# Performance work log

Measured on AMD Instinct MI355X. Metric: run time of the kernel, lower is better.

Reference implementation:

```python
import jax, jax.numpy as jnp
import numpy as np

B, S, H, L, NH, OUT = 64, 512, 512, 2, 8, 1
HD = H // NH
SKIP_INTERVAL = 2
EPS = 1e-5


def ln(x, g, b):
    m = x.mean(-1, keepdims=True)
    v = x.var(-1, keepdims=True)
    return (x - m) / jnp.sqrt(v + EPS) * g + b


def setup_inputs() -> dict:
    key = jax.random.key(0)
    ks = iter(jax.random.split(key, 64))
    def nrm(shape, s=0.02):
        return jax.random.normal(next(ks), shape, jnp.float32) * s
    inp = {
        'x': jax.random.normal(next(ks), (B, S, H), jnp.float32),
        # stacked per-layer LSTM params (input_size == hidden_size == H)
        'Wi': nrm((L, 4 * H, H)), 'bi': jnp.zeros((L, 4 * H), jnp.float32).at[:, H:2 * H].set(1.0),
        'Wh': nrm((L, 4 * H, H)), 'bh': jnp.zeros((L, 4 * H), jnp.float32).at[:, H:2 * H].set(1.0),
        'g_in': jnp.ones((L, 4 * H), jnp.float32), 'b_in': jnp.zeros((L, 4 * H), jnp.float32),
        'g_hid': jnp.ones((L, 4 * H), jnp.float32), 'b_hid': jnp.zeros((L, 4 * H), jnp.float32),
        'g_cell': jnp.ones((L, H), jnp.float32), 'b_cell': jnp.zeros((L, H), jnp.float32),
        # highway per layer
        'hw_Wt': nrm((L, H, H)), 'hw_bt': jnp.zeros((L, H), jnp.float32),
        'hw_Wc': nrm((L, H, H)), 'hw_bc': jnp.full((L, H), -1.0, jnp.float32),
        'hw_Wh': nrm((L, H, H)), 'hw_bh': jnp.zeros((L, H), jnp.float32),
        # attention
        'Wq': nrm((H, H)), 'bq': jnp.zeros((H,), jnp.float32),
        'Wk': nrm((H, H)), 'bk': jnp.zeros((H,), jnp.float32),
        'Wv': nrm((H, H)), 'bv': jnp.zeros((H,), jnp.float32),
        'Wo': nrm((H, H)), 'bo': jnp.zeros((H,), jnp.float32),
        'att_g': jnp.ones((H,), jnp.float32), 'att_b': jnp.zeros((H,), jnp.float32),
        # output norm + projection head
        'on_g': jnp.ones((H,), jnp.float32), 'on_b': jnp.zeros((H,), jnp.float32),
        'Wp1': nrm((H // 2, H)), 'bp1': jnp.zeros((H // 2,), jnp.float32),
        'Wp2': nrm((OUT, H // 2)), 'bp2': jnp.zeros((OUT,), jnp.float32),
    }
    return inp


def _forward(x, Wi, bi, Wh, bh, g_in, b_in, g_hid, b_hid, g_cell, b_cell,
             hw_Wt, hw_bt, hw_Wc, hw_bc, hw_Wh, hw_bh,
             Wq, bq, Wk, bk, Wv, bv, Wo, bo, att_g, att_b,
             on_g, on_b, Wp1, bp1, Wp2, bp2):
    def lstm_layer(seq, l):
        # precompute input projection + its LayerNorm for all timesteps: [B,S,4H]
        ip = ln(jnp.einsum('bsh,gh->bsg', seq, Wi[l]) + bi[l], g_in[l], b_in[l])
        def step(carry, ip_t):
            h, c = carry
            hp = ln(h @ Wh[l].T + bh[l], g_hid[l], b_hid[l])
            i_, f_, g_, o_ = jnp.split(ip_t + hp, 4, axis=-1)
            c = jax.nn.sigmoid(f_) * c + jax.nn.sigmoid(i_) * jnp.tanh(g_)
            h = jax.nn.sigmoid(o_) * jnp.tanh(ln(c, g_cell[l], b_cell[l]))
            return (h, c), h
        h0 = jnp.zeros((seq.shape[0], H), seq.dtype)
        _, hs = jax.lax.scan(step, (h0, h0), jnp.swapaxes(ip, 0, 1))
        return jnp.swapaxes(hs, 0, 1)  # [B,S,H]

    seq = x
    for l in range(L):
        h_seq = lstm_layer(seq, l)
        # highway network
        tg = jax.nn.sigmoid(h_seq @ hw_Wt[l].T + hw_bt[l])
        cg = jax.nn.sigmoid(h_seq @ hw_Wc[l].T + hw_bc[l])
        tr = jax.nn.relu(h_seq @ hw_Wh[l].T + hw_bh[l])
        h_seq = tg * tr + cg * h_seq
        # skip connection every SKIP_INTERVAL layers
        if l > 0 and (l + 1) % SKIP_INTERVAL == 0:
            h_seq = h_seq + seq
        seq = h_seq

    # multi-head self-attention with residual + LayerNorm
    def heads(y):
        return jnp.swapaxes(y.reshape(B, S, NH, HD), 1, 2)  # [B,NH,S,HD]
    q = heads(seq @ Wq.T + bq)
    k = heads(seq @ Wk.T + bk)
    v = heads(seq @ Wv.T + bv)
    scale = 1.0 / float(np.sqrt(HD))
    scores = jnp.einsum('bnqd,bnkd->bnqk', q, k) * scale
    aw = jax.nn.softmax(scores, axis=-1)
    ctx = jnp.einsum('bnqk,bnkd->bnqd', aw, v)
    ctx = jnp.swapaxes(ctx, 1, 2).reshape(B, S, H)
    att = ln(ctx @ Wo.T + bo + seq, att_g, att_b)

    # last timestep -> output norm -> MLP head
    last = ln(att[:, -1], on_g, on_b)
    hmid = jax.nn.relu(last @ Wp1.T + bp1)
    return hmid @ Wp2.T + bp2  # [B, OUT]


def reference(x, Wi, bi, Wh, bh, g_in, b_in, g_hid, b_hid, g_cell, b_cell,
              hw_Wt, hw_bt, hw_Wc, hw_bc, hw_Wh, hw_bh,
              Wq, bq, Wk, bk, Wv, bv, Wo, bo, att_g, att_b,
              on_g, on_b, Wp1, bp1, Wp2, bp2):
    return _forward(x, Wi, bi, Wh, bh, g_in, b_in, g_hid, b_hid, g_cell, b_cell,
                    hw_Wt, hw_bt, hw_Wc, hw_bc, hw_Wh, hw_bh,
                    Wq, bq, Wk, bk, Wv, bv, Wo, bo, att_g, att_b,
                    on_g, on_b, Wp1, bp1, Wp2, bp2)
```

## Files before the change

kernel.cpp:

```cpp
#include <hip/hip_runtime.h>

#define EPS_LN 1e-5f

static constexpr int Bn  = 64;
static constexpr int Sn  = 512;
static constexpr int Hn  = 512;
static constexpr int G4n = 2048;

typedef unsigned int uint32;
typedef unsigned long long uint64;
typedef _Float16 h2v __attribute__((ext_vector_type(2)));

__device__ __forceinline__ float sigf(float x)     { return 1.0f / (1.0f + __expf(-x)); }
__device__ __forceinline__ float tanhfast(float x) { return 1.0f - 2.0f / (1.0f + __expf(2.0f * x)); }

__device__ __forceinline__ float dot2h(uint32 w, uint32 h, float acc) {
#if defined(__has_builtin)
#if __has_builtin(__builtin_amdgcn_fdot2)
  return __builtin_amdgcn_fdot2(__builtin_bit_cast(h2v, w), __builtin_bit_cast(h2v, h), acc, false);
#define DOT2_DONE 1
#endif
#endif
#ifndef DOT2_DONE
  h2v wv = __builtin_bit_cast(h2v, w);
  h2v hv = __builtin_bit_cast(h2v, h);
  return acc + (float)wv.x * (float)hv.x + (float)wv.y * (float)hv.y;
#endif
}
__device__ __forceinline__ uint32 packh2(float a, float b) {
  h2v v; v.x = (_Float16)a; v.y = (_Float16)b;
  return __builtin_bit_cast(uint32, v);
}

__device__ __forceinline__ float blk_sum(float v, float* sm, int tid) {
#pragma unroll
  for (int o = 32; o; o >>= 1) v += __shfl_down(v, o, 64);
  __syncthreads();
  if ((tid & 63) == 0) sm[tid >> 6] = v;
  __syncthreads();
  return sm[0] + sm[1] + sm[2] + sm[3];
}
__device__ __forceinline__ float blk_max(float v, float* sm, int tid) {
#pragma unroll
  for (int o = 32; o; o >>= 1) v = fmaxf(v, __shfl_down(v, o, 64));
  __syncthreads();
  if ((tid & 63) == 0) sm[tid >> 6] = v;
  __syncthreads();
  return fmaxf(fmaxf(sm[0], sm[1]), fmaxf(sm[2], sm[3]));
}

__device__ __forceinline__ void blk_sum4_w8(float& a, float& b, float& c, float& d,
                                            float* sm, int tid) {
#pragma unroll
  for (int o = 32; o; o >>= 1) {
    a += __shfl_down(a, o, 64);
    b += __shfl_down(b, o, 64);
    c += __shfl_down(c, o, 64);
    d += __shfl_down(d, o, 64);
  }
  __syncthreads();
  if ((tid & 63) == 0) {
    float4 v; v.x = a; v.y = b; v.z = c; v.w = d;
    *(float4*)&sm[(tid >> 6) * 4] = v;
  }
  __syncthreads();
  float ra = 0.f, rb = 0.f, rc = 0.f, rd = 0.f;
#pragma unroll
  for (int w = 0; w < 8; ++w) {
    float4 v = *(const float4*)&sm[w * 4];
    ra += v.x; rb += v.y; rc += v.z; rd += v.w;
  }
  a = ra; b = rb; c = rc; d = rd;
}

__global__ __launch_bounds__(256) void wh_pack_k(
    const float* __restrict__ Wh, uint32* __restrict__ WhP)
{
  __shared__ float tile[32][33];
  const int l = blockIdx.z;
  const int k0 = blockIdx.x * 32;
  const int n0 = blockIdx.y * 32;
  const int row = threadIdx.x >> 5, col = threadIdx.x & 31;
  const float* src = Wh + (long)l * G4n * Hn;
  uint32* dst = WhP + (long)l * 256 * G4n;
#pragma unroll
  for (int rr = 0; rr < 4; ++rr) {
    int nn = row + rr * 8;
    tile[nn][col] = src[(long)(n0 + nn) * Hn + k0 + col];
  }
  __syncthreads();
#pragma unroll
  for (int rr = 0; rr < 2; ++rr) {
    int kpl = row + rr * 8;
    int kp = (k0 >> 1) + kpl;
    dst[(long)kp * G4n + n0 + col] = packh2(tile[col][2*kpl], tile[col][2*kpl+1]);
  }
}

__global__ void init_zbuf_k(uint64* zbuf)
{
  long i = (long)blockIdx.x * 512 + threadIdx.x;
  zbuf[i] = 0ULL;
}

__global__ __launch_bounds__(256) void gemm_ip_k(
    const float* __restrict__ A,
    const float* __restrict__ Bw,
    const float* __restrict__ bias,
    float* __restrict__ C,
    int s0)
{
  __shared__ __align__(16) uint32 Ah[8][128];
  __shared__ __align__(16) uint32 Bh[8][128];
  const int tid = threadIdx.x;
  const long m0 = (long)blockIdx.y * 128;
  const long n0 = (long)blockIdx.x * 128;
  const int tx = tid & 15, ty = tid >> 4;
  const int lrow = tid >> 1;
  const int lc0  = (tid & 1) * 8;
  const int kb   = (tid & 1) * 4;
  float acc[8][8];
#pragma unroll
  for (int i = 0; i < 8; ++i)
#pragma unroll
    for (int j = 0; j < 8; ++j) acc[i][j] = 0.f;

  const long r  = m0 + lrow;
  const long b  = r & 63;
  const long sl = r >> 6;
  const float* Arow = A + (b * Sn + s0 + sl) * Hn;
  const float* Brow = Bw + (n0 + lrow) * 512L;

  float4 a0 = *(const float4*)(Arow + lc0);
  float4 a1 = *(const float4*)(Arow + lc0 + 4);
  float4 b0 = *(const float4*)(Brow + lc0);
  float4 b1 = *(const float4*)(Brow + lc0 + 4);

  for (int k0 = 0; k0 < 512; k0 += 16) {
    __syncthreads();
    Ah[kb+0][lrow] = packh2(a0.x, a0.y);
    Ah[kb+1][lrow] = packh2(a0.z, a0.w);
    Ah[kb+2][lrow] = packh2(a1.x, a1.y);
    Ah[kb+3][lrow] = packh2(a1.z, a1.w);
    Bh[kb+0][lrow] = packh2(b0.x, b0.y);
    Bh[kb+1][lrow] = packh2(b0.z, b0.w);
    Bh[kb+2][lrow] = packh2(b1.x, b1.y);
    Bh[kb+3][lrow] = packh2(b1.z, b1.w);
    __syncthreads();
    if (k0 + 16 < 512) {
      a0 = *(const float4*)(Arow + k0 + 16 + lc0);
      a1 = *(const float4*)(Arow + k0 + 16 + lc0 + 4);
      b0 = *(const float4*)(Brow + k0 + 16 + lc0);
      b1 = *(const float4*)(Brow + k0 + 16 + lc0 + 4);
    }
#pragma unroll
    for (int kp = 0; kp < 8; ++kp) {
      uint32 a8[8], b8[8];
      *(uint4*)&a8[0] = *(const uint4*)&Ah[kp][ty*8];
      *(uint4*)&a8[4] = *(const uint4*)&Ah[kp][ty*8+4];
      *(uint4*)&b8[0] = *(const uint4*)&Bh[kp][tx*8];
      *(uint4*)&b8[4] = *(const uint4*)&Bh[kp][tx*8+4];
#pragma unroll
      for (int i = 0; i < 8; ++i)
#pragma unroll
        for (int j = 0; j < 8; ++j) acc[i][j] = dot2h(a8[i], b8[j], acc[i][j]);
    }
  }
#pragma unroll
  for (int i = 0; i < 8; ++i) {
    long m = m0 + ty*8 + i;
    float* crow = C + m * 2048L + n0 + tx*8;
    const float* br = bias + n0 + tx*8;
    float4 o0, o1;
    o0.x = acc[i][0]+br[0]; o0.y = acc[i][1]+br[1]; o0.z = acc[i][2]+br[2]; o0.w = acc[i][3]+br[3];
    o1.x = acc[i][4]+br[4]; o1.y = acc[i][5]+br[5]; o1.z = acc[i][6]+br[6]; o1.w = acc[i][7]+br[7];
    *(float4*)crow = o0; *(float4*)(crow+4) = o1;
  }
}

__global__ __launch_bounds__(256) void hw_fused_k(
    const float* __restrict__ A,
    const float* __restrict__ Wt, const float* __restrict__ bt,
    const float* __restrict__ Wc, const float* __restrict__ bc,
    const float* __restrict__ Wh3, const float* __restrict__ bh3,
    float* __restrict__ seqout,
    int skip)
{
  __shared__ __align__(16) uint32 Ah[8][128];
  __shared__ __align__(16) uint32 Bh[3][8][68];
  const int tid = threadIdx.x;
  const long m0 = (long)blockIdx.y * 128;
  const int n0 = blockIdx.x * 64;
  const int tx = tid & 7;
  const int ty = tid >> 3;
  const int lrow = tid >> 1;
  const int lc0  = (tid & 1) * 8;
  const int kbA  = (tid & 1) * 4;
  const int brow = tid >> 2;
  const int bk0  = (tid & 3) * 4;
  const int kbB  = (tid & 3) * 2;

  float accT[4][8], accC[4][8], accH[4][8];
#pragma unroll
  for (int i = 0; i < 4; ++i)
#pragma unroll
    for (int j = 0; j < 8; ++j) { accT[i][j] = 0.f; accC[i][j] = 0.f; accH[i][j] = 0.f; }

  const float* Arow = A + (m0 + lrow) * 512;
  const long boff = (long)(n0 + brow) * 512 + bk0;

  float4 a0 = *(const float4*)(Arow + lc0);
  float4 a1 = *(const float4*)(Arow + lc0 + 4);
  float4 wt4 = *(const float4*)(Wt  + boff);
  float4 wc4 = *(const float4*)(Wc  + boff);
  float4 wh4 = *(const float4*)(Wh3 + boff);

  for (int k0 = 0; k0 < 512; k0 += 16) {
    __syncthreads();
    Ah[kbA+0][lrow] = packh2(a0.x, a0.y);
    Ah[kbA+1][lrow] = packh2(a0.z, a0.w);
    Ah[kbA+2][lrow] = packh2(a1.x, a1.y);
    Ah[kbA+3][lrow] = packh2(a1.z, a1.w);
    Bh[0][kbB+0][brow] = packh2(wt4.x, wt4.y);
    Bh[0][kbB+1][brow] = packh2(wt4.z, wt4.w);
    Bh[1][kbB+0][brow] = packh2(wc4.x, wc4.y);
    Bh[1][kbB+1][brow] = packh2(wc4.z, wc4.w);
    Bh[2][kbB+0][brow] = packh2(wh4.x, wh4.y);
    Bh[2][kbB+1][brow] = packh2(wh4.z, wh4.w);
    __syncthreads();
    if (k0 + 16 < 512) {
      a0 = *(const float4*)(Arow + k0 + 16 + lc0);
      a1 = *(const float4*)(Arow + k0 + 16 + lc0 + 4);
      wt4 = *(const float4*)(Wt  + boff + k0 + 16);
      wc4 = *(const float4*)(Wc  + boff + k0 + 16);
      wh4 = *(const float4*)(Wh3 + boff + k0 + 16);
    }
#pragma unroll
    for (int kp = 0; kp < 8; ++kp) {
      uint32 a4[4];
      *(uint4*)&a4[0] = *(const uint4*)&Ah[kp][ty*4];
      {
        uint32 b8[8];
        *(uint4*)&b8[0] = *(const uint4*)&Bh[0][kp][tx*8];
        *(uint4*)&b8[4] = *(const uint4*)&Bh[0][kp][tx*8+4];
#pragma unroll
        for (int i = 0; i < 4; ++i)
#pragma unroll
          for (int j = 0; j < 8; ++j) accT[i][j] = dot2h(a4[i], b8[j], accT[i][j]);
      }
      {
        uint32 b8[8];
        *(uint4*)&b8[0] = *(const uint4*)&Bh[1][kp][tx*8];
        *(uint4*)&b8[4] = *(const uint4*)&Bh[1][kp][tx*8+4];
#pragma unroll
        for (int i = 0; i < 4; ++i)
#pragma unroll
          for (int j = 0; j < 8; ++j) accC[i][j] = dot2h(a4[i], b8[j], accC[i][j]);
      }
      {
        uint32 b8[8];
        *(uint4*)&b8[0] = *(const uint4*)&Bh[2][kp][tx*8];
        *(uint4*)&b8[4] = *(const uint4*)&Bh[2][kp][tx*8+4];
#pragma unroll
        for (int i = 0; i < 4; ++i)
#pragma unroll
          for (int j = 0; j < 8; ++j) accH[i][j] = dot2h(a4[i], b8[j], accH[i][j]);
      }
    }
  }

  float btr[8], bcr[8], bhr[8];
#pragma unroll
  for (int j = 0; j < 8; ++j) {
    btr[j] = bt[n0 + tx*8 + j];
    bcr[j] = bc[n0 + tx*8 + j];
    bhr[j] = bh3[n0 + tx*8 + j];
  }
#pragma unroll
  for (int i = 0; i < 4; ++i) {
    const long m = m0 + ty*4 + i;
    const float* hrow = A + m * 512 + n0 + tx*8;
    float* srow = seqout + m * 512 + n0 + tx*8;
    float4 h0 = *(const float4*)hrow;
    float4 h1 = *(const float4*)(hrow + 4);
    float hv[8] = {h0.x,h0.y,h0.z,h0.w,h1.x,h1.y,h1.z,h1.w};
    float sv[8] = {0,0,0,0,0,0,0,0};
    if (skip) {
      float4 s0 = *(const float4*)srow;
      float4 s1 = *(const float4*)(srow + 4);
      sv[0]=s0.x; sv[1]=s0.y; sv[2]=s0.z; sv[3]=s0.w;
      sv[4]=s1.x; sv[5]=s1.y; sv[6]=s1.z; sv[7]=s1.w;
    }
    float o[8];
#pragma unroll
    for (int j = 0; j < 8; ++j) {
      const float t1 = accT[i][j] + btr[j];
      const float t2 = accC[i][j] + bcr[j];
      const float t3 = accH[i][j] + bhr[j];
      o[j] = sigf(t1) * fmaxf(t3, 0.f) + sigf(t2) * hv[j] + sv[j];
    }
    float4 o0, o1;
    o0.x=o[0]; o0.y=o[1]; o0.z=o[2]; o0.w=o[3];
    o1.x=o[4]; o1.y=o[5]; o1.z=o[6]; o1.w=o[7];
    *(float4*)srow = o0; *(float4*)(srow + 4) = o1;
  }
}

__global__ __launch_bounds__(256) void gemm_m64_k(
    const float* __restrict__ A, long lda,
    const float* __restrict__ Bw,
    const float* __restrict__ bias,
    float* __restrict__ P,
    int N, int K)
{
  __shared__ float As[64][64];
  __shared__ float Bs[64][64];
  const int tid = threadIdx.x;
  const int n0 = blockIdx.x * 64;
  const int kc = blockIdx.y;
  const int Kc = K / gridDim.y;
  const int tx = tid & 15, ty = tid >> 4;
  const int row = tid >> 2, q = tid & 3;
  float acc[4][4];
#pragma unroll
  for (int i = 0; i < 4; ++i)
#pragma unroll
    for (int j = 0; j < 4; ++j) acc[i][j] = 0.f;

  for (int k0 = kc * Kc; k0 < kc * Kc + Kc; k0 += 64) {
    float4 a[4], b[4];
#pragma unroll
    for (int c = 0; c < 4; ++c) {
      a[c] = *(const float4*)(A  + (long)row * lda       + k0 + q*16 + c*4);
      b[c] = *(const float4*)(Bw + (long)(n0 + row) * K  + k0 + q*16 + c*4);
    }
    __syncthreads();
#pragma unroll
    for (int c = 0; c < 4; ++c) {
      int kb = q*16 + c*4;
      As[kb+0][row]=a[c].x; As[kb+1][row]=a[c].y; As[kb+2][row]=a[c].z; As[kb+3][row]=a[c].w;
      Bs[kb+0][row]=b[c].x; Bs[kb+1][row]=b[c].y; Bs[kb+2][row]=b[c].z; Bs[kb+3][row]=b[c].w;
    }
    __syncthreads();
#pragma unroll
    for (int kk = 0; kk < 64; ++kk) {
      float4 av = *(const float4*)&As[kk][ty*4];
      float4 bv = *(const float4*)&Bs[kk][tx*4];
      float am[4] = {av.x, av.y, av.z, av.w};
      float bm[4] = {bv.x, bv.y, bv.z, bv.w};
#pragma unroll
      for (int i = 0; i < 4; ++i)
#pragma unroll
        for (int j = 0; j < 4; ++j) acc[i][j] += am[i] * bm[j];
    }
  }
#pragma unroll
  for (int i = 0; i < 4; ++i) {
    int m = ty*4 + i;
    float* pr = P + ((long)kc * 64 + m) * N + n0 + tx*4;
#pragma unroll
    for (int j = 0; j < 4; ++j) {
      float bb = bias ? bias[n0 + tx*4 + j] : 0.f;
      pr[j] = acc[i][j] + bb;
    }
  }
}

__global__ __launch_bounds__(512, 2) void lstm_seqz_k(
    const uint32* __restrict__ WhP,
    const float* __restrict__ bh,
    const float* __restrict__ ipc,
    const float* __restrict__ g_hid, const float* __restrict__ b_hid,
    const float* __restrict__ g_cell, const float* __restrict__ b_cell,
    float* __restrict__ hst, float* __restrict__ cst,
    float* __restrict__ hseq,
    uint64* __restrict__ zbuf,
    int t0, int nsteps, int gbase)
{
  const int blk = blockIdx.x;
  const int g   = blk & 31;
  const int kq  = blk >> 5;
  const int tid = threadIdx.x;
  const int b0  = g*2, b1 = g*2 + 1;
  const int r   = tid >> 1;
  const int kh  = tid & 1;
  __shared__ __align__(16) uint32 hp0[264];
  __shared__ __align__(16) uint32 hp1[264];
  __shared__ float sm[32];

  uint4 wreg[32];
  {
    const uint32* base = WhP + (long)(kh * 128) * 2048 + (kq*256 + r);
#pragma unroll
    for (int i = 0; i < 32; ++i) {
      wreg[i].x = base[(long)(4*i + 0) * 2048];
      wreg[i].y = base[(long)(4*i + 1) * 2048];
      wreg[i].z = base[(long)(4*i + 2) * 2048];
      wreg[i].w = base[(long)(4*i + 3) * 2048];
    }
  }

  float bhr[4], ghr[4], bhir[4];
#pragma unroll
  for (int q = 0; q < 4; ++q) {
    bhr[q]  = bh[q*512 + tid];
    ghr[q]  = g_hid[q*512 + tid];
    bhir[q] = b_hid[q*512 + tid];
  }
  const float gcv = g_cell[tid];
  const float bcv = b_cell[tid];
  float c0 = cst[b0*512 + tid];
  float c1 = cst[b1*512 + tid];
  float h0 = hst[b0*512 + tid];
  float h1 = hst[b1*512 + tid];

  {
    const float p0 = __shfl_xor(h0, 1, 64);
    const float p1 = __shfl_xor(h1, 1, 64);
    if (!(tid & 1)) {
      const int j = tid >> 1;
      const int jj = (j < 128) ? j : j + 4;
      hp0[jj] = packh2(h0, p0);
      hp1[jj] = packh2(h1, p1);
    }
  }
  __syncthreads();

  const long myword = (long)(kq*256 + r) * 2 + kh;
  const uint32* hb0 = hp0 + kh * 132;
  const uint32* hb1 = hp1 + kh * 132;

  for (int ts = 0; ts < nsteps; ++ts) {
    const int gstep = gbase + ts;
    const uint32 tagw = (uint32)gstep;
    uint64* zp = zbuf + (long)(gstep & 1) * 131072 + (long)g * 4096;

    const float* iprow0 = ipc + ((long)ts * 64 + b0) * 2048 + tid;
    const float* iprow1 = ipc + ((long)ts * 64 + b1) * 2048 + tid;
    float ip0[4], ip1[4];
#pragma unroll
    for (int q = 0; q < 4; ++q) { ip0[q] = iprow0[q*512]; ip1[q] = iprow1[q*512]; }

    float a0 = 0.f, a1 = 0.f;
#pragma unroll
    for (int i = 0; i < 32; ++i) {
      const uint4 w  = wreg[i];
      const uint4 hv0 = *(const uint4*)&hb0[4*i];
      const uint4 hv1 = *(const uint4*)&hb1[4*i];
      a0 = dot2h(w.x, hv0.x, a0); a0 = dot2h(w.y, hv0.y, a0);
      a0 = dot2h(w.z, hv0.z, a0); a0 = dot2h(w.w, hv0.w, a0);
      a1 = dot2h(w.x, hv1.x, a1); a1 = dot2h(w.y, hv1.y, a1);
      a1 = dot2h(w.z, hv1.z, a1); a1 = dot2h(w.w, hv1.w, a1);
    }
    a0 += __shfl_xor(a0, 1, 64);
    a1 += __shfl_xor(a1, 1, 64);

    {
      const float zval = kh ? a1 : a0;
      const uint64 w = ((uint64)tagw << 32) | (uint64)__builtin_bit_cast(uint32, zval);
      __hip_atomic_store(zp + myword, w, __ATOMIC_RELAXED, __HIP_MEMORY_SCOPE_AGENT);
    }

    float z0[4], z1[4];
    {
      uint64 v0[4], v1[4];
      int pend = 0xff;
      while (pend) {
#pragma unroll
        for (int q = 0; q < 4; ++q) {
          const long base = (long)(q*512 + tid) * 2;
          if (pend & (1 << q)) {
            uint64 w = __hip_atomic_load(zp + base, __ATOMIC_RELAXED, __HIP_MEMORY_SCOPE_AGENT);
            if ((uint32)(w >> 32) == tagw) { v0[q] = w; pend &= ~(1 << q); }
          }
          if (pend & (16 << q)) {
            uint64 w = __hip_atomic_load(zp + base + 1, __ATOMIC_RELAXED, __HIP_MEMORY_SCOPE_AGENT);
            if ((uint32)(w >> 32) == tagw) { v1[q] = w; pend &= ~(16 << q); }
          }
        }
        if (pend) __builtin_amdgcn_s_sleep(2);
      }
#pragma unroll
      for (int q = 0; q < 4; ++q) {
        z0[q] = __builtin_bit_cast(float, (uint32)v0[q]) + bhr[q];
        z1[q] = __builtin_bit_cast(float, (uint32)v1[q]) + bhr[q];
      }
    }

    float s10 = z0[0]+z0[1]+z0[2]+z0[3];
    float s20 = z0[0]*z0[0] + z0[1]*z0[1] + z0[2]*z0[2] + z0[3]*z0[3];
    float s11 = z1[0]+z1[1]+z1[2]+z1[3];
    float s21 = z1[0]*z1[0] + z1[1]*z1[1] + z1[2]*z1[2] + z1[3]*z1[3];
    blk_sum4_w8(s10, s20, s11, s21, sm, tid);
    const float m0 = s10 * (1.f/2048.f);
    const float r0 = rsqrtf(s20 * (1.f/2048.f) - m0*m0 + EPS_LN);
    const float m1 = s11 * (1.f/2048.f);
    const float r1 = rsqrtf(s21 * (1.f/2048.f) - m1*m1 + EPS_LN);

    const float gi0 = ip0[0] + (z0[0] - m0) * r0 * ghr[0] + bhir[0];
    const float gf0 = ip0[1] + (z0[1] - m0) * r0 * ghr[1] + bhir[1];
    const float gg0 = ip0[2] + (z0[2] - m0) * r0 * ghr[2] + bhir[2];
    const float go0 = ip0[3] + (z0[3] - m0) * r0 * ghr[3] + bhir[3];
    const float gi1 = ip1[0] + (z1[0] - m1) * r1 * ghr[0] + bhir[0];
    const float gf1 = ip1[1] + (z1[1] - m1) * r1 * ghr[1] + bhir[1];
    const float gg1 = ip1[2] + (z1[2] - m1) * r1 * ghr[2] + bhir[2];
    const float go1 = ip1[3] + (z1[3] - m1) * r1 * ghr[3] + bhir[3];

    c0 = sigf(gf0) * c0 + sigf(gi0) * tanhfast(gg0);
    c1 = sigf(gf1) * c1 + sigf(gi1) * tanhfast(gg1);

    float t10 = c0, t20 = c0*c0, t11 = c1, t21 = c1*c1;
    blk_sum4_w8(t10, t20, t11, t21, sm, tid);
    const float n0 = t10 * (1.f/512.f);
    const float q0r = rsqrtf(t20 * (1.f/512.f) - n0*n0 + EPS_LN);
    const float n1 = t11 * (1.f/512.f);
    const float q1r = rsqrtf(t21 * (1.f/512.f) - n1*n1 + EPS_LN);
    h0 = sigf(go0) * tanhfast((c0 - n0) * q0r * gcv + bcv);
    h1 = sigf(go1) * tanhfast((c1 - n1) * q1r * gcv + bcv);

    if (kq == 0) {
      hseq[((long)b0 * Sn + t0 + ts) * Hn + tid] = h0;
      hseq[((long)b1 * Sn + t0 + ts) * Hn + tid] = h1;
    }

    const float p0 = __shfl_xor(h0, 1, 64);
    const float p1 = __shfl_xor(h1, 1, 64);
    if (!(tid & 1)) {
      const int j = tid >> 1;
      const int jj = (j < 128) ? j : j + 4;
      hp0[jj] = packh2(h0, p0);
      hp1[jj] = packh2(h1, p1);
    }
    __syncthreads();
  }
  if (kq == 0) {
    hst[b0*512 + tid] = h0; hst[b1*512 + tid] = h1;
    cst[b0*512 + tid] = c0; cst[b1*512 + tid] = c1;
  }
}

__global__ __launch_bounds__(256) void ln_rows_k(
    float* __restrict__ X, const float* __restrict__ g, const float* __restrict__ bt)
{
  const long row = blockIdx.x;
  float* xr = X + row * 2048L;
  const int tid = threadIdx.x;
  __shared__ float sm[4];
  float4 v0 = *(float4*)(xr + tid*8);
  float4 v1 = *(float4*)(xr + tid*8 + 4);
  float s1 = v0.x+v0.y+v0.z+v0.w + v1.x+v1.y+v1.z+v1.w;
  float s2 = v0.x*v0.x+v0.y*v0.y+v0.z*v0.z+v0.w*v0.w
           + v1.x*v1.x+v1.y*v1.y+v1.z*v1.z+v1.w*v1.w;
  s1 = blk_sum(s1, sm, tid);
  s2 = blk_sum(s2, sm, tid);
  const float mean = s1 * (1.f/2048.f);
  const float rstd = rsqrtf(s2 * (1.f/2048.f) - mean*mean + EPS_LN);
  const int base = tid*8;
  float vals[8] = {v0.x,v0.y,v0.z,v0.w,v1.x,v1.y,v1.z,v1.w};
#pragma unroll
  for (int c = 0; c < 8; ++c)
    xr[base + c] = (vals[c] - mean) * rstd * g[base + c] + bt[base + c];
}

__global__ void init_hc_k(float* h, float* c)
{
  int i = blockIdx.x * 256 + threadIdx.x;
  h[i] = 0.f; c[i] = 0.f;
}

__global__ __launch_bounds__(256) void qkh_k(
    const float* __restrict__ qlst, const float* __restrict__ Wk,
    const float* __restrict__ bk,
    float* __restrict__ qkh, float* __restrict__ qbk)
{
  const int hd = blockIdx.x, cg = blockIdx.y;
  const int b = threadIdx.x & 63, sc = threadIdx.x >> 6;
  const int col0 = cg * 128 + sc * 32;
  float qreg[64];
  const float* qp = qlst + b*512 + hd*64;
#pragma unroll
  for (int j4 = 0; j4 < 16; ++j4) {
    float4 v = *(const float4*)(qp + j4*4);
    qreg[j4*4+0]=v.x; qreg[j4*4+1]=v.y; qreg[j4*4+2]=v.z; qreg[j4*4+3]=v.w;
  }
  float acc[32];
#pragma unroll
  for (int c = 0; c < 32; ++c) acc[c] = 0.f;
  for (int j = 0; j < 64; ++j) {
    float qv = qreg[j];
    const float* wr = Wk + (long)(hd*64 + j)*512 + col0;
#pragma unroll
    for (int c4 = 0; c4 < 8; ++c4) {
      float4 w = *(const float4*)(wr + c4*4);
      acc[c4*4+0] = __builtin_fmaf(qv, w.x, acc[c4*4+0]);
      acc[c4*4+1] = __builtin_fmaf(qv, w.y, acc[c4*4+1]);
      acc[c4*4+2] = __builtin_fmaf(qv, w.z, acc[c4*4+2]);
      acc[c4*4+3] = __builtin_fmaf(qv, w.w, acc[c4*4+3]);
    }
  }
  float* op = qkh + ((long)b*8 + hd)*512 + col0;
#pragma unroll
  for (int c4 = 0; c4 < 8; ++c4) {
    float4 o;
    o.x = acc[c4*4+0]; o.y = acc[c4*4+1]; o.z = acc[c4*4+2]; o.w = acc[c4*4+3];
    *(float4*)(op + c4*4) = o;
  }
  if (cg == 0 && sc == 0) {
    float s = 0.f;
    for (int j = 0; j < 64; ++j) s += qreg[j] * bk[hd*64 + j];
    qbk[b*8 + hd] = s;
  }
}

__global__ __launch_bounds__(256) void attn2_k(
    const float* __restrict__ seq,
    const float* __restrict__ qkh,
    const float* __restrict__ qbk,
    float* __restrict__ u)
{
  const int b = blockIdx.x, hd = blockIdx.y, tid = threadIdx.x;
  __shared__ __align__(16) float qk[512];
  __shared__ float p[512];
  __shared__ float sm[4];
  qk[tid]       = qkh[((long)b*8 + hd)*512 + tid];
  qk[tid + 256] = qkh[((long)b*8 + hd)*512 + tid + 256];
  __syncthreads();
  const float bias = qbk[b*8 + hd];

  float loc[2]; float mx = -3.0e38f;
#pragma unroll
  for (int v = 0; v < 2; ++v) {
    int s = tid + v*256;
    const float4* sr = (const float4*)(seq + ((long)b*512 + s)*512);
    const float4* qv4 = (const float4*)qk;
    float d = 0.f;
    for (int k4 = 0; k4 < 128; ++k4) {
      float4 sv = sr[k4], qv = qv4[k4];
      d += sv.x*qv.x + sv.y*qv.y + sv.z*qv.z + sv.w*qv.w;
    }
    d = (d + bias) * 0.125f;
    loc[v] = d; mx = fmaxf(mx, d);
  }
  const float M = blk_max(mx, sm, tid);
  float sum = 0.f;
#pragma unroll
  for (int v = 0; v < 2; ++v) {
    int s = tid + v*256;
    float e = __expf(loc[v] - M);
    p[s] = e; sum += e;
  }
  const float SM = blk_sum(sum, sm, tid);
  const float inv = 1.f / SM;

  float u0 = 0.f, u1 = 0.f;
  for (int s = 0; s < 512; ++s) {
    float ps = p[s];
    const float* srow = seq + ((long)b*512 + s)*512;
    u0 = __builtin_fmaf(ps, srow[tid], u0);
    u1 = __builtin_fmaf(ps, srow[tid + 256], u1);
  }
  u[((long)b*8 + hd)*512 + tid]       = u0 * inv;
  u[((long)b*8 + hd)*512 + tid + 256] = u1 * inv;
}

__global__ __launch_bounds__(256) void ctxv_k(
    const float* __restrict__ u, const float* __restrict__ Wv,
    const float* __restrict__ bv, float* __restrict__ ctx)
{
  const int b = blockIdx.x, tid = threadIdx.x;
  __shared__ __align__(16) float ul[8*512];
  for (int i = tid; i < 4096; i += 256) ul[i] = u[(long)b*4096 + i];
  __syncthreads();
#pragma unroll
  for (int v = 0; v < 2; ++v) {
    int n = tid + v*256;
    int hd = n >> 6;
    const float4* wr = (const float4*)(Wv + (long)n*512);
    const float4* uv = (const float4*)&ul[hd*512];
    float acc = 0.f;
    for (int k4 = 0; k4 < 128; ++k4) {
      float4 w = wr[k4], x = uv[k4];
      acc += w.x*x.x + w.y*x.y + w.z*x.z + w.w*x.w;
    }
    ctx[b*512 + n] = acc + bv[n];
  }
}

__global__ __launch_bounds__(256) void head_k(
    const float* __restrict__ ctx,
    const float* __restrict__ Wo, const float* __restrict__ bo,
    const float* __restrict__ seq,
    const float* __restrict__ att_g, const float* __restrict__ att_b,
    const float* __restrict__ on_g, const float* __restrict__ on_b,
    const float* __restrict__ Wp1, const float* __restrict__ bp1,
    const float* __restrict__ Wp2, const float* __restrict__ bp2,
    float* __restrict__ out)
{
  const int b = blockIdx.x, tid = threadIdx.x;
  __shared__ __align__(16) float cs[512];
  __shared__ __align__(16) float buf[512];
  __shared__ float sm[4];
  cs[tid]       = ctx[b*512 + tid];
  cs[tid + 256] = ctx[b*512 + tid + 256];
  __syncthreads();

  const float* srow = seq + ((long)b*512 + 511) * 512;
  float o[2];
#pragma unroll
  for (int v = 0; v < 2; ++v) {
    int j = tid + v*256;
    const float4* w4 = (const float4*)(Wo + (long)j * 512);
    const float4* c4 = (const float4*)cs;
    float acc = 0.f;
    for (int kx = 0; kx < 128; ++kx) {
      float4 w = w4[kx], c = c4[kx];
      acc += w.x*c.x + w.y*c.y + w.z*c.z + w.w*c.w;
    }
    o[v] = acc + bo[j] + srow[j];
  }
  float s1 = o[0] + o[1], s2 = o[0]*o[0] + o[1]*o[1];
  s1 = blk_sum(s1, sm, tid); s2 = blk_sum(s2, sm, tid);
  float m1 = s1 * (1.f/512.f);
  float r1 = rsqrtf(s2 * (1.f/512.f) - m1*m1 + EPS_LN);
  float a[2];
#pragma unroll
  for (int v = 0; v < 2; ++v) {
    int j = tid + v*256;
    a[v] = (o[v] - m1) * r1 * att_g[j] + att_b[j];
  }
  s1 = a[0] + a[1]; s2 = a[0]*a[0] + a[1]*a[1];
  s1 = blk_sum(s1, sm, tid); s2 = blk_sum(s2, sm, tid);
  float m2 = s1 * (1.f/512.f);
  float r2 = rsqrtf(s2 * (1.f/512.f) - m2*m2 + EPS_LN);
#pragma unroll
  for (int v = 0; v < 2; ++v) {
    int j = tid + v*256;
    buf[j] = (a[v] - m2) * r2 * on_g[j] + on_b[j];
  }
  __syncthreads();

  const float4* w1 = (const float4*)(Wp1 + (long)tid * 512);
  const float4* b4 = (const float4*)buf;
  float acc = 0.f;
  for (int kx = 0; kx < 128; ++kx) {
    float4 w = w1[kx], c = b4[kx];
    acc += w.x*c.x + w.y*c.y + w.z*c.z + w.w*c.w;
  }
  float mid = fmaxf(acc + bp1[tid], 0.f);
  float contrib = mid * Wp2[tid];
  float tot = blk_sum(contrib, sm, tid);
  if (tid == 0) out[b] = tot + bp2[0];
}

extern "C" void kernel_launch(void* const* d_in, const int* in_sizes, int n_in,
                              void* d_out, int out_size, void* d_ws, size_t ws_size,
                              hipStream_t stream)
{
  const float* x     = (const float*)d_in[0];
  const float* Wi    = (const float*)d_in[1];
  const float* bi    = (const float*)d_in[2];
  const float* Wh    = (const float*)d_in[3];
  const float* bh    = (const float*)d_in[4];
  const float* g_in  = (const float*)d_in[5];
  const float* b_in  = (const float*)d_in[6];
  const float* g_hid = (const float*)d_in[7];
  const float* b_hid = (const float*)d_in[8];
  const float* g_cell= (const float*)d_in[9];
  const float* b_cell= (const float*)d_in[10];
  const float* hwWt  = (const float*)d_in[11];
  const float* hwbt  = (const float*)d_in[12];
  const float* hwWc  = (const float*)d_in[13];
  const float* hwbc  = (const float*)d_in[14];
  const float* hwWh  = (const float*)d_in[15];
  const float* hwbh  = (const float*)d_in[16];
  const float* Wq    = (const float*)d_in[17];
  const float* bq    = (const float*)d_in[18];
  const float* Wk    = (const float*)d_in[19];
  const float* bk    = (const float*)d_in[20];
  const float* Wv    = (const float*)d_in[21];
  const float* bv    = (const float*)d_in[22];
  const float* Wo    = (const float*)d_in[23];
  const float* bo    = (const float*)d_in[24];
  const float* att_g = (const float*)d_in[25];
  const float* att_b = (const float*)d_in[26];
  const float* on_g  = (const float*)d_in[27];
  const float* on_b  = (const float*)d_in[28];
  const float* Wp1   = (const float*)d_in[29];
  const float* bp1   = (const float*)d_in[30];
  const float* Wp2   = (const float*)d_in[31];
  const float* bp2   = (const float*)d_in[32];
  float* out = (float*)d_out;

  const long SEQF = (long)Bn * Sn * Hn;
  const long WHPF = 2L * 256 * G4n;
  const long ZBF  = 2L * 32 * 2048 * 2;
  const long wsF  = (long)(ws_size / 4);

  float* ws   = (float*)d_ws;
  float* seq  = ws;
  float* hseq = seq  + SEQF;
  uint32* WhP = (uint32*)(hseq + SEQF);
  uint64* zbuf = (uint64*)(hseq + SEQF + WHPF);
  float* hst  = hseq + SEQF + WHPF + 2*ZBF;
  float* cst  = hst  + 32768L;
  float* qlst = cst  + 32768L;
  float* ctx  = qlst + 32768L;
  float* qkh  = ctx  + 32768L;
  float* qbk  = qkh  + 262144L;
  float* uat  = qbk  + 1024L;
  float* ipc  = uat  + 262144L;
  const long baseF = (ipc - ws);

  int TCH = 128;
  while (TCH > 16 && baseF + (long)TCH * 64 * 2048 > wsF) TCH >>= 1;

  wh_pack_k<<<dim3(16, 64, 2), 256, 0, stream>>>(Wh, WhP);
  init_zbuf_k<<<512, 512, 0, stream>>>(zbuf);

  const int NCH = Sn / TCH;
  const int MROWS = TCH * 64;
  const int NMCH = (Bn * Sn) / MROWS;

  for (int l = 0; l < 2; ++l) {
    const float* seqin = (l == 0) ? x : seq;
    init_hc_k<<<128, 256, 0, stream>>>(hst, cst);
    for (int c = 0; c < NCH; ++c) {
      const int s0 = c * TCH;
      gemm_ip_k<<<dim3(16, TCH/2), 256, 0, stream>>>(seqin, Wi + (long)l*G4n*Hn, bi + l*G4n, ipc, s0);
      ln_rows_k<<<TCH*64, 256, 0, stream>>>(ipc, g_in + l*G4n, b_in + l*G4n);
      lstm_seqz_k<<<256, 512, 0, stream>>>(WhP + (long)l*256*G4n, bh + l*G4n, ipc,
          g_hid + l*G4n, b_hid + l*G4n, g_cell + l*Hn, b_cell + l*Hn,
          hst, cst, hseq, zbuf, s0, TCH, l*Sn + s0 + 1);
    }
    for (int mc = 0; mc < NMCH; ++mc) {
      const long m0 = (long)mc * MROWS;
      hw_fused_k<<<dim3(8, MROWS/128), 256, 0, stream>>>(
          hseq + m0*512,
          hwWt + (long)l*Hn*Hn, hwbt + l*Hn,
          hwWc + (long)l*Hn*Hn, hwbc + l*Hn,
          hwWh + (long)l*Hn*Hn, hwbh + l*Hn,
          seq + m0*512, (l == 0) ? 0 : 1);
    }
  }

  gemm_m64_k<<<dim3(8, 1), 256, 0, stream>>>(seq + 511L*512, 512L*512, Wq, bq, qlst, 512, 512);
  qkh_k<<<dim3(8, 4), 256, 0, stream>>>(qlst, Wk, bk, qkh, qbk);
  attn2_k<<<dim3(64, 8), 256, 0, stream>>>(seq, qkh, qbk, uat);
  ctxv_k<<<64, 256, 0, stream>>>(uat, Wv, bv, ctx);
  head_k<<<64, 256, 0, stream>>>(ctx, Wo, bo, seq, att_g, att_b, on_g, on_b, Wp1, bp1, Wp2, bp2, out);
}
```

Measured before the change: 9.184 ms.

## Store input projection as fp16 and apply input LayerNorm inside LSTM kernel

The input-projection GEMM now writes packed fp16 pairs instead of fp32. The separate LayerNorm pass is replaced by a stats-only kernel that writes a per-row mean and rstd. The recurrent LSTM kernel reads the fp16 values and applies the normalization with g_in/b_in inline, which removes a full read-modify-write pass and halves the per-step loads of the projection buffer. The smaller buffer also lets the time chunk grow to 256, so there are fewer chunk launches, at the cost of fp16 rounding of pre-normalization gate inputs.

Measured after the change: 9.067 ms. About the same (-1.3%).

```diff
diff --git a/kernel.cpp b/kernel.cpp
--- a/kernel.cpp
+++ b/kernel.cpp
@@ -107,7 +107,7 @@
     const float* __restrict__ A,
     const float* __restrict__ Bw,
     const float* __restrict__ bias,
-    float* __restrict__ C,
+    uint32* __restrict__ C,
     int s0)
 {
   __shared__ __align__(16) uint32 Ah[8][128];
@@ -169,12 +169,41 @@
 #pragma unroll
   for (int i = 0; i < 8; ++i) {
     long m = m0 + ty*8 + i;
-    float* crow = C + m * 2048L + n0 + tx*8;
+    uint32* crow = C + m * 1024 + (n0 >> 1) + tx*4;
     const float* br = bias + n0 + tx*8;
-    float4 o0, o1;
-    o0.x = acc[i][0]+br[0]; o0.y = acc[i][1]+br[1]; o0.z = acc[i][2]+br[2]; o0.w = acc[i][3]+br[3];
-    o1.x = acc[i][4]+br[4]; o1.y = acc[i][5]+br[5]; o1.z = acc[i][6]+br[6]; o1.w = acc[i][7]+br[7];
-    *(float4*)crow = o0; *(float4*)(crow+4) = o1;
+    uint4 o;
+    o.x = packh2(acc[i][0]+br[0], acc[i][1]+br[1]);
+    o.y = packh2(acc[i][2]+br[2], acc[i][3]+br[3]);
+    o.z = packh2(acc[i][4]+br[4], acc[i][5]+br[5]);
+    o.w = packh2(acc[i][6]+br[6], acc[i][7]+br[7]);
+    *(uint4*)crow = o;
+  }
+}
+
+__global__ __launch_bounds__(256) void ipstats_k(
+    const uint32* __restrict__ X, float* __restrict__ st)
+{
+  const long row = blockIdx.x;
+  const uint32* xr = X + row * 1024;
+  const int tid = threadIdx.x;
+  __shared__ float sm[4];
+  uint4 w = *(const uint4*)(xr + tid*4);
+  h2v a = __builtin_bit_cast(h2v, w.x);
+  h2v b = __builtin_bit_cast(h2v, w.y);
+  h2v c = __builtin_bit_cast(h2v, w.z);
+  h2v d = __builtin_bit_cast(h2v, w.w);
+  float v[8] = {(float)a.x,(float)a.y,(float)b.x,(float)b.y,
+                (float)c.x,(float)c.y,(float)d.x,(float)d.y};
+  float s1 = 0.f, s2 = 0.f;
+#pragma unroll
+  for (int i = 0; i < 8; ++i) { s1 += v[i]; s2 += v[i]*v[i]; }
+  s1 = blk_sum(s1, sm, tid);
+  s2 = blk_sum(s2, sm, tid);
+  if (tid == 0) {
+    const float mean = s1 * (1.f/2048.f);
+    const float rstd = rsqrtf(s2 * (1.f/2048.f) - mean*mean + EPS_LN);
+    st[row*2]     = mean;
+    st[row*2 + 1] = rstd;
   }
 }
 
@@ -369,7 +398,9 @@
 __global__ __launch_bounds__(512, 2) void lstm_seqz_k(
     const uint32* __restrict__ WhP,
     const float* __restrict__ bh,
-    const float* __restrict__ ipc,
+    const uint32* __restrict__ ipc,
+    const float* __restrict__ ipstats,
+    const float* __restrict__ g_in, const float* __restrict__ b_in,
     const float* __restrict__ g_hid, const float* __restrict__ b_hid,
     const float* __restrict__ g_cell, const float* __restrict__ b_cell,
     float* __restrict__ hst, float* __restrict__ cst,
@@ -400,12 +431,14 @@
     }
   }
 
-  float bhr[4], ghr[4], bhir[4];
+  float bhr[4], ghr[4], bhir[4], ginr[4], binr[4];
 #pragma unroll
   for (int q = 0; q < 4; ++q) {
     bhr[q]  = bh[q*512 + tid];
     ghr[q]  = g_hid[q*512 + tid];
     bhir[q] = b_hid[q*512 + tid];
+    ginr[q] = g_in[q*512 + tid];
+    binr[q] = b_in[q*512 + tid];
   }
   const float gcv = g_cell[tid];
   const float bcv = b_cell[tid];
@@ -435,11 +468,20 @@
     const uint32 tagw = (uint32)gstep;
     uint64* zp = zbuf + (long)(gstep & 1) * 131072 + (long)g * 4096;
 
-    const float* iprow0 = ipc + ((long)ts * 64 + b0) * 2048 + tid;
-    const float* iprow1 = ipc + ((long)ts * 64 + b1) * 2048 + tid;
+    const uint32* iprow0 = ipc + ((long)ts * 64 + b0) * 1024 + (tid >> 1);
+    const uint32* iprow1 = ipc + ((long)ts * 64 + b1) * 1024 + (tid >> 1);
+    const float2 st0 = *(const float2*)(ipstats + ((long)ts * 64 + b0) * 2);
+    const float2 st1 = *(const float2*)(ipstats + ((long)ts * 64 + b1) * 2);
     float ip0[4], ip1[4];
 #pragma unroll
-    for (int q = 0; q < 4; ++q) { ip0[q] = iprow0[q*512]; ip1[q] = iprow1[q*512]; }
+    for (int q = 0; q < 4; ++q) {
+      h2v v0 = __builtin_bit_cast(h2v, iprow0[q*256]);
+      h2v v1 = __builtin_bit_cast(h2v, iprow1[q*256]);
+      const float r0 = kh ? (float)v0.y : (float)v0.x;
+      const float r1 = kh ? (float)v1.y : (float)v1.x;
+      ip0[q] = (r0 - st0.x) * st0.y * ginr[q] + binr[q];
+      ip1[q] = (r1 - st1.x) * st1.y * ginr[q] + binr[q];
+    }
 
     float a0 = 0.f, a1 = 0.f;
 #pragma unroll
@@ -537,29 +579,6 @@
     hst[b0*512 + tid] = h0; hst[b1*512 + tid] = h1;
     cst[b0*512 + tid] = c0; cst[b1*512 + tid] = c1;
   }
-}
-
-__global__ __launch_bounds__(256) void ln_rows_k(
-    float* __restrict__ X, const float* __restrict__ g, const float* __restrict__ bt)
-{
-  const long row = blockIdx.x;
-  float* xr = X + row * 2048L;
-  const int tid = threadIdx.x;
-  __shared__ float sm[4];
-  float4 v0 = *(float4*)(xr + tid*8);
-  float4 v1 = *(float4*)(xr + tid*8 + 4);
-  float s1 = v0.x+v0.y+v0.z+v0.w + v1.x+v1.y+v1.z+v1.w;
-  float s2 = v0.x*v0.x+v0.y*v0.y+v0.z*v0.z+v0.w*v0.w
-           + v1.x*v1.x+v1.y*v1.y+v1.z*v1.z+v1.w*v1.w;
-  s1 = blk_sum(s1, sm, tid);
-  s2 = blk_sum(s2, sm, tid);
-  const float mean = s1 * (1.f/2048.f);
-  const float rstd = rsqrtf(s2 * (1.f/2048.f) - mean*mean + EPS_LN);
-  const int base = tid*8;
-  float vals[8] = {v0.x,v0.y,v0.z,v0.w,v1.x,v1.y,v1.z,v1.w};
-#pragma unroll
-  for (int c = 0; c < 8; ++c)
-    xr[base + c] = (vals[c] - mean) * rstd * g[base + c] + bt[base + c];
 }
 
 __global__ void init_hc_k(float* h, float* c)
@@ -808,11 +827,13 @@
   float* qkh  = ctx  + 32768L;
   float* qbk  = qkh  + 262144L;
   float* uat  = qbk  + 1024L;
-  float* ipc  = uat  + 262144L;
-  const long baseF = (ipc - ws);
-
-  int TCH = 128;
-  while (TCH > 16 && baseF + (long)TCH * 64 * 2048 > wsF) TCH >>= 1;
+  float* ipstats = uat + 262144L;
+  float* ipcF = ipstats + 32768L;
+  uint32* ipc = (uint32*)ipcF;
+  const long baseF = (ipcF - ws);
+
+  int TCH = 256;
+  while (TCH > 16 && baseF + (long)TCH * 64 * 1024 > wsF) TCH >>= 1;
 
   wh_pack_k<<<dim3(16, 64, 2), 256, 0, stream>>>(Wh, WhP);
   init_zbuf_k<<<512, 512, 0, stream>>>(zbuf);
@@ -827,8 +848,9 @@
     for (int c = 0; c < NCH; ++c) {
       const int s0 = c * TCH;
       gemm_ip_k<<<dim3(16, TCH/2), 256, 0, stream>>>(seqin, Wi + (long)l*G4n*Hn, bi + l*G4n, ipc, s0);
-      ln_rows_k<<<TCH*64, 256, 0, stream>>>(ipc, g_in + l*G4n, b_in + l*G4n);
-      lstm_seqz_k<<<256, 512, 0, stream>>>(WhP + (long)l*256*G4n, bh + l*G4n, ipc,
+      ipstats_k<<<TCH*64, 256, 0, stream>>>(ipc, ipstats);
+      lstm_seqz_k<<<256, 512, 0, stream>>>(WhP + (long)l*256*G4n, bh + l*G4n, ipc, ipstats,
+          g_in + l*G4n, b_in + l*G4n,
           g_hid + l*G4n, b_hid + l*G4n, g_cell + l*Hn, b_cell + l*Hn,
           hst, cst, hseq, zbuf, s0, TCH, l*Sn + s0 + 1);
     }
```
